# Kernel tuning notes

Measured on AMD Instinct MI355X. Metric: run time of the kernel, lower is better.

The kernel has to match this reference:

```python
import jax, jax.numpy as jnp
import numpy as np

NUM_LAYER = 6
NUM_HEADS = 1
NEG_INF = -1e9


def setup_inputs() -> dict:
    key = jax.random.key(0)
    ks = jax.random.split(key, 8)
    bs, C, N = 8, 128, 2048
    H0 = (jax.random.uniform(ks[0], (bs, N, N)) < 0.2).astype(jnp.float32)
    vertex_feat = jax.random.normal(ks[1], (bs, C, N), dtype=jnp.float32)
    edge_feat = jax.random.normal(ks[2], (bs, C, N), dtype=jnp.float32)
    s = 1.0 / np.sqrt(C)  # Conv1d(k=1) default init scale
    Wq = jax.random.uniform(ks[3], (C, C), minval=-s, maxval=s, dtype=jnp.float32)
    bq = jax.random.uniform(ks[4], (C,), minval=-s, maxval=s, dtype=jnp.float32)
    Wk = jax.random.uniform(ks[5], (C, C), minval=-s, maxval=s, dtype=jnp.float32)
    bk = jax.random.uniform(ks[6], (C,), minval=-s, maxval=s, dtype=jnp.float32)
    return {"H0": H0, "vertex_feat": vertex_feat, "edge_feat": edge_feat,
            "Wq": Wq, "bq": bq, "Wk": Wk, "bk": bk, "it": 4}


def reference(H0, vertex_feat, edge_feat, Wq, bq, Wk, bk, it):
    bs, N, _ = H0.shape
    C = Wq.shape[0]
    head = NUM_HEADS
    dh = C // head
    # Conv1d kernel_size=1 == pointwise linear over channel dim
    Q = (jnp.einsum('oc,bcn->bon', Wq, vertex_feat) + bq[None, :, None]).reshape(bs, head, dh, N)
    K = (jnp.einsum('oc,bcn->bon', Wk, edge_feat) + bk[None, :, None]).reshape(bs, head, dh, N)
    att = jnp.einsum('bhco,bhci->bhoi', Q, K) / np.sqrt(dh)  # [bs,h,N,N]
    mask = jnp.where(H0 > 0, 0.0, NEG_INF)                   # masked_fill(1-H0)
    score = jax.nn.sigmoid(att + mask[:, None]).sum(axis=1) / head  # [bs,N,N]
    # mask_score, choice='topk': keep top-k scores per row
    k = round(N * 0.1 * (NUM_LAYER - 1 - it))
    topk_vals = jax.lax.top_k(score, k)[0]          # [bs,N,k]
    a_min = topk_vals[..., -1:]                     # k-th largest per row
    W = jnp.where(score >= a_min, score, 0.0)
    H = jnp.where(W > 0, H0, 0.0)
    # degree-normalization matrices (diag_embed of 1/deg, inf -> 0)
    deg_E = H.sum(axis=1)   # [bs,N] edge degrees
    deg_V = H.sum(axis=2)   # [bs,N] vertex degrees
    De_n_1 = jax.vmap(jnp.diag)(jnp.where(deg_E != 0, 1.0 / deg_E, 0.0))
    Dv_n_1 = jax.vmap(jnp.diag)(jnp.where(deg_V != 0, 1.0 / deg_V, 0.0))
    # edge weights: L2-normalized column sums of W (F.normalize, eps=1e-12)
    W_edge = W.sum(axis=1)
    nrm = jnp.maximum(jnp.linalg.norm(W_edge, axis=1, keepdims=True), 1e-12)
    W_edge = (W_edge / nrm)[:, :, None]  # [bs,N,1]
    return H, W, De_n_1, Dv_n_1, W_edge
```

## Files before the change

### kernel.cpp

```cpp
#include <hip/hip_runtime.h>
#include <math.h>

#define NUM_LAYER 6

typedef __attribute__((ext_vector_type(8))) short short8;
typedef __attribute__((ext_vector_type(4))) float f32x4;
typedef unsigned short u16;

__device__ __forceinline__ void split3(float x, u16& h, u16& m, u16& l) {
  unsigned ux = __float_as_uint(x);
  h = (u16)(ux >> 16);
  float r1 = x - __uint_as_float(ux & 0xFFFF0000u);
  unsigned u1 = __float_as_uint(r1);
  m = (u16)(u1 >> 16);
  float r2 = r1 - __uint_as_float(u1 & 0xFFFF0000u);
  l = (u16)(__float_as_uint(r2) >> 16);
}

__global__ __launch_bounds__(256) void qk_gemm_split(
    const float* __restrict__ Wq, const float* __restrict__ bq,
    const float* __restrict__ vf,
    const float* __restrict__ Wk, const float* __restrict__ bk,
    const float* __restrict__ ef,
    u16* __restrict__ Qh, u16* __restrict__ Qm, u16* __restrict__ Ql,
    u16* __restrict__ Kh, u16* __restrict__ Km, u16* __restrict__ Kl,
    int C, int N, int bs) {
  int which = (int)blockIdx.y >= bs;
  int b = (int)blockIdx.y - (which ? bs : 0);
  const float* Wm = which ? Wk : Wq;
  const float* bias = which ? bk : bq;
  const float* X = (which ? ef : vf) + (size_t)b * C * N;
  u16* Ph = which ? Kh : Qh;
  u16* Pm = which ? Km : Qm;
  u16* Pl = which ? Kl : Ql;
  int n0 = blockIdx.x * 128;
  __shared__ float As[8][128];
  __shared__ float Xs[8][128];
  int t = threadIdx.x;
  int tx = t & 15, ty = t >> 4;
  int ao = t >> 1, ac = (t & 1) * 4;
  int lk = t >> 5, lj = (t & 31) * 4;
  float acc[8][8] = {};
  for (int c0 = 0; c0 < C; c0 += 8) {
    __syncthreads();
    float4 wv = *(const float4*)&Wm[(size_t)ao * C + c0 + ac];
    As[ac + 0][ao] = wv.x; As[ac + 1][ao] = wv.y;
    As[ac + 2][ao] = wv.z; As[ac + 3][ao] = wv.w;
    *(float4*)&Xs[lk][lj] = *(const float4*)&X[(size_t)(c0 + lk) * N + n0 + lj];
    __syncthreads();
#pragma unroll
    for (int kk = 0; kk < 8; ++kk) {
      float a[8], bb[8];
      *(float4*)&a[0]  = *(const float4*)&As[kk][ty * 4];
      *(float4*)&a[4]  = *(const float4*)&As[kk][64 + ty * 4];
      *(float4*)&bb[0] = *(const float4*)&Xs[kk][tx * 4];
      *(float4*)&bb[4] = *(const float4*)&Xs[kk][64 + tx * 4];
#pragma unroll
      for (int i = 0; i < 8; ++i)
#pragma unroll
        for (int j = 0; j < 8; ++j)
          acc[i][j] = fmaf(a[i], bb[j], acc[i][j]);
    }
  }
  float bv[8];
#pragma unroll
  for (int i = 0; i < 8; ++i) bv[i] = bias[(i >> 2) * 64 + ty * 4 + (i & 3)];
#pragma unroll
  for (int j = 0; j < 8; ++j) {
    int n = n0 + tx * 4 + (j & 3) + (j >> 2) * 64;
    size_t nb = ((size_t)b * N + n) * C;
#pragma unroll
    for (int g = 0; g < 2; ++g) {
      int r0 = g * 64 + ty * 4;
      ushort4 hv, mv, lv;
      split3(acc[g * 4 + 0][j] + bv[g * 4 + 0], hv.x, mv.x, lv.x);
      split3(acc[g * 4 + 1][j] + bv[g * 4 + 1], hv.y, mv.y, lv.y);
      split3(acc[g * 4 + 2][j] + bv[g * 4 + 2], hv.z, mv.z, lv.z);
      split3(acc[g * 4 + 3][j] + bv[g * 4 + 3], hv.w, mv.w, lv.w);
      *(ushort4*)&Ph[nb + r0] = hv;
      *(ushort4*)&Pm[nb + r0] = mv;
      *(ushort4*)&Pl[nb + r0] = lv;
    }
  }
}

__global__ __launch_bounds__(256) void att_mfma(
    const u16* __restrict__ Qh, const u16* __restrict__ Qm,
    const u16* __restrict__ Ql, const u16* __restrict__ Kh,
    const u16* __restrict__ Km, const u16* __restrict__ Kl,
    const float* __restrict__ H0, float* __restrict__ score,
    int C, int N, float rsdh) {
  int b = blockIdx.z;
  int o0 = blockIdx.y * 128, i0 = blockIdx.x * 128;
  __shared__ u16 sm[6][128][40];
  __shared__ float et[4][16][68];
  int t = threadIdx.x;
  int wave = t >> 6, lane = t & 63, quad = lane >> 4, lr = lane & 15;
  int wo = wave >> 1, wi = wave & 1;
  f32x4 acc[4][4];
#pragma unroll
  for (int mi = 0; mi < 4; ++mi)
#pragma unroll
    for (int ni = 0; ni < 4; ++ni) acc[mi][ni] = (f32x4){0.f, 0.f, 0.f, 0.f};

  int ro = t >> 1, ch = (t & 1) * 16;
  size_t qbase = ((size_t)b * N + o0 + ro) * C + ch;
  size_t kbase = ((size_t)b * N + i0 + ro) * C + ch;
  const u16* gq[3] = {Qh, Qm, Ql};
  const u16* gk[3] = {Kh, Km, Kl};

  for (int c0 = 0; c0 < C; c0 += 32) {
    __syncthreads();
#pragma unroll
    for (int a = 0; a < 3; ++a) {
      const uint4* src = (const uint4*)(gq[a] + qbase + c0);
      *(uint4*)&sm[a][ro][ch] = src[0];
      *(uint4*)&sm[a][ro][ch + 8] = src[1];
      const uint4* srk = (const uint4*)(gk[a] + kbase + c0);
      *(uint4*)&sm[3 + a][ro][ch] = srk[0];
      *(uint4*)&sm[3 + a][ro][ch + 8] = srk[1];
    }
    __syncthreads();
    short8 bh[4], bm[4], bl[4];
#pragma unroll
    for (int ni = 0; ni < 4; ++ni) {
      int row = wi * 64 + ni * 16 + lr;
      bh[ni] = *(const short8*)&sm[3][row][quad * 8];
      bm[ni] = *(const short8*)&sm[4][row][quad * 8];
      bl[ni] = *(const short8*)&sm[5][row][quad * 8];
    }
#pragma unroll
    for (int mi = 0; mi < 4; ++mi) {
      int row = wo * 64 + mi * 16 + lr;
      short8 ah = *(const short8*)&sm[0][row][quad * 8];
      short8 am = *(const short8*)&sm[1][row][quad * 8];
      short8 al = *(const short8*)&sm[2][row][quad * 8];
#pragma unroll
      for (int ni = 0; ni < 4; ++ni) {
        f32x4 c = acc[mi][ni];
        c = __builtin_amdgcn_mfma_f32_16x16x32_bf16(ah, bl[ni], c, 0, 0, 0);
        c = __builtin_amdgcn_mfma_f32_16x16x32_bf16(al, bh[ni], c, 0, 0, 0);
        c = __builtin_amdgcn_mfma_f32_16x16x32_bf16(am, bm[ni], c, 0, 0, 0);
        c = __builtin_amdgcn_mfma_f32_16x16x32_bf16(ah, bm[ni], c, 0, 0, 0);
        c = __builtin_amdgcn_mfma_f32_16x16x32_bf16(am, bh[ni], c, 0, 0, 0);
        c = __builtin_amdgcn_mfma_f32_16x16x32_bf16(ah, bh[ni], c, 0, 0, 0);
        acc[mi][ni] = c;
      }
    }
  }
  const float* Hb = H0 + (size_t)b * N * N;
  float* Sb = score + (size_t)b * N * N;
  int rr = lane >> 2, seg = lane & 3;
#pragma unroll
  for (int mi = 0; mi < 4; ++mi) {
#pragma unroll
    for (int ni = 0; ni < 4; ++ni)
#pragma unroll
      for (int r = 0; r < 4; ++r)
        et[wave][quad * 4 + r][ni * 16 + lr] = acc[mi][ni][r];
    __syncthreads();
    int o = o0 + wo * 64 + mi * 16 + rr;
    const float* hr = Hb + (size_t)o * N + i0 + wi * 64;
    float* sr = Sb + (size_t)o * N + i0 + wi * 64;
#pragma unroll
    for (int j = 0; j < 4; ++j) {
      int col = j * 16 + seg * 4;
      float4 c = *(const float4*)&et[wave][rr][col];
      float4 h = *(const float4*)&hr[col];
      float4 oV;
      oV.x = (h.x > 0.f) ? 1.f / (1.f + __expf(-c.x * rsdh)) : 0.f;
      oV.y = (h.y > 0.f) ? 1.f / (1.f + __expf(-c.y * rsdh)) : 0.f;
      oV.z = (h.z > 0.f) ? 1.f / (1.f + __expf(-c.z * rsdh)) : 0.f;
      oV.w = (h.w > 0.f) ? 1.f / (1.f + __expf(-c.w * rsdh)) : 0.f;
      *(float4*)&sr[col] = oV;
    }
    __syncthreads();
  }
}

template <int NQ>
__global__ __launch_bounds__(512) void select_wh_t(
    const float* __restrict__ H0, float* __restrict__ scoreW,
    float* __restrict__ Hout, float* __restrict__ degV,
    float* __restrict__ PE, float* __restrict__ PW,
    const int* __restrict__ itp, int N) {
  int b = blockIdx.y;
  int strip = blockIdx.x;
  int r0 = strip * 8;
  int t = threadIdx.x;
  int wave = t >> 6, lane = t & 63;
  size_t bNN = (size_t)b * N * N;
  __shared__ float aminS[8];
  __shared__ float dpart[8][8];

  {
    int row = r0 + wave;
    const float* srow = scoreW + bNN + (size_t)row * N;
    float v[NQ];
#pragma unroll
    for (int q = 0; q < NQ; ++q) v[q] = srow[lane + (q << 6)];
    int itv = *itp;
    int k = (int)floor((double)N * 0.1 * (double)(NUM_LAYER - 1 - itv) + 0.5);
    unsigned lo = 0u, hi = 0x3F800000u;
    while (lo < hi) {
      unsigned mid = lo + ((hi - lo + 1u) >> 1);
      float thr = __uint_as_float(mid);
      int c = 0;
#pragma unroll
      for (int q = 0; q < NQ; ++q) c += (v[q] >= thr) ? 1 : 0;
#pragma unroll
      for (int off = 1; off < 64; off <<= 1) c += __shfl_xor(c, off);
      if (c >= k) lo = mid; else hi = mid - 1u;
    }
    if (lane == 0) aminS[wave] = __uint_as_float(lo);
  }
  __syncthreads();

  float4 accE = {0.f, 0.f, 0.f, 0.f};
  float4 accW = {0.f, 0.f, 0.f, 0.f};
  float dv[8];
#pragma unroll
  for (int r = 0; r < 8; ++r) {
    float am = aminS[r];
    size_t off = bNN + (size_t)(r0 + r) * N + 4 * t;
    float4 s  = *(const float4*)(scoreW + off);
    float4 h0 = *(const float4*)(H0 + off);
    float4 w, h;
    w.x = (s.x >= am) ? s.x : 0.f; h.x = (w.x > 0.f) ? h0.x : 0.f;
    w.y = (s.y >= am) ? s.y : 0.f; h.y = (w.y > 0.f) ? h0.y : 0.f;
    w.z = (s.z >= am) ? s.z : 0.f; h.z = (w.z > 0.f) ? h0.z : 0.f;
    w.w = (s.w >= am) ? s.w : 0.f; h.w = (w.w > 0.f) ? h0.w : 0.f;
    *(float4*)(scoreW + off) = w;
    *(float4*)(Hout + off) = h;
    accW.x += w.x; accW.y += w.y; accW.z += w.z; accW.w += w.w;
    accE.x += h.x; accE.y += h.y; accE.z += h.z; accE.w += h.w;
    dv[r] = h.x + h.y + h.z + h.w;
  }
#pragma unroll
  for (int r = 0; r < 8; ++r) {
    float x = dv[r];
#pragma unroll
    for (int off = 32; off; off >>= 1) x += __shfl_down(x, off);
    if (lane == 0) dpart[wave][r] = x;
  }
  __syncthreads();
  if (t < 8) {
    float s = 0.f;
#pragma unroll
    for (int w = 0; w < 8; ++w) s += dpart[w][t];
    degV[b * N + r0 + t] = s;
  }
  int S = N >> 3;
  size_t pbase = ((size_t)b * S + strip) * N + 4 * t;
  *(float4*)(PE + pbase) = accE;
  *(float4*)(PW + pbase) = accW;
}

__global__ __launch_bounds__(256) void col_reduce(
    const float* __restrict__ PE, const float* __restrict__ PW,
    float* __restrict__ degE, float* __restrict__ We, int N, int S) {
  int b = blockIdx.y;
  int col = blockIdx.x * 256 + threadIdx.x;
  float se0 = 0.f, se1 = 0.f, sw0 = 0.f, sw1 = 0.f;
  for (int s = 0; s < S; s += 2) {
    size_t off0 = ((size_t)b * S + s) * N + col;
    size_t off1 = off0 + N;
    se0 += PE[off0]; se1 += PE[off1];
    sw0 += PW[off0]; sw1 += PW[off1];
  }
  degE[b * N + col] = se0 + se1;
  We[b * N + col] = sw0 + sw1;
}

__global__ __launch_bounds__(256) void dedv_fill(
    float* __restrict__ De, float* __restrict__ Dv,
    const float* __restrict__ degE, const float* __restrict__ degV, int N) {
  int arr = blockIdx.z;
  int b = blockIdx.y;
  int r0 = blockIdx.x * 8;
  float* out = (arr ? Dv : De) + (size_t)b * N * N;
  const float* deg = (arr ? degV : degE) + b * N;
  int t = threadIdx.x;
#pragma unroll
  for (int r = r0; r < r0 + 8; ++r) {
    float d = deg[r];
    float inv = (d != 0.f) ? 1.f / d : 0.f;
    size_t rowoff = (size_t)r * N;
    for (int c4 = t * 4; c4 < N; c4 += 1024) {
      float4 v = {0.f, 0.f, 0.f, 0.f};
      unsigned dd = (unsigned)(r - c4);
      if (dd < 4u) ((float*)&v)[dd] = inv;
      *(float4*)&out[rowoff + c4] = v;
    }
  }
}

__global__ __launch_bounds__(256) void wedge_norm(
    const float* __restrict__ We, float* __restrict__ out, int N) {
  int b = blockIdx.x;
  int t = threadIdx.x;
  const float* w = We + (size_t)b * N;
  float ss = 0.f;
  for (int i = t; i < N; i += 256) { float x = w[i]; ss += x * x; }
  for (int off = 32; off; off >>= 1) ss += __shfl_down(ss, off);
  __shared__ float p[4];
  if ((t & 63) == 0) p[t >> 6] = ss;
  __syncthreads();
  float tot = p[0] + p[1] + p[2] + p[3];
  float nrm = fmaxf(sqrtf(tot), 1e-12f);
  for (int i = t; i < N; i += 256) out[(size_t)b * N + i] = w[i] / nrm;
}

extern "C" void kernel_launch(void* const* d_in, const int* in_sizes, int n_in,
                              void* d_out, int out_size, void* d_ws, size_t ws_size,
                              hipStream_t stream) {
  const float* H0 = (const float*)d_in[0];
  const float* vf = (const float*)d_in[1];
  const float* ef = (const float*)d_in[2];
  const float* Wq = (const float*)d_in[3];
  const float* bq = (const float*)d_in[4];
  const float* Wk = (const float*)d_in[5];
  const float* bk = (const float*)d_in[6];
  const int* itp  = (const int*)d_in[7];

  int C = (int)(sqrt((double)in_sizes[3]) + 0.5);
  long long ratio = (long long)in_sizes[0] / in_sizes[1];
  int N = (int)(C * ratio);
  int bs = (int)(in_sizes[1] / ((long long)C * N));
  size_t bNN = (size_t)bs * N * N;
  size_t bNC = (size_t)bs * N * C;
  int S = N >> 3;
  size_t pElems = (size_t)bs * S * N;

  float* outH  = (float*)d_out;
  float* outW  = outH + bNN;
  float* outDe = outW + bNN;
  float* outDv = outDe + bNN;
  float* outWe = outDv + bNN;

  size_t bsN = (size_t)bs * N;
  float* degE = (float*)d_ws;
  float* degV = degE + bsN;
  float* We   = degV + bsN;
  u16* splits;
  float* PE;
  float* PW;
  size_t need = 3 * bsN * sizeof(float) + 6 * bNC * sizeof(u16) +
                2 * pElems * sizeof(float);
  if (ws_size >= need) {
    splits = (u16*)(We + bsN);
    PE = (float*)(splits + 6 * bNC);
    PW = PE + pElems;
  } else {
    splits = (u16*)outDe;
    PE = outDv;
    PW = PE + pElems;
  }
  u16* Qh = splits;
  u16* Qm = Qh + bNC;
  u16* Ql = Qm + bNC;
  u16* Kh = Ql + bNC;
  u16* Km = Kh + bNC;
  u16* Kl = Km + bNC;

  float rsdh = (float)(1.0 / sqrt((double)C));

  qk_gemm_split<<<dim3(N / 128, 2 * bs), 256, 0, stream>>>(
      Wq, bq, vf, Wk, bk, ef, Qh, Qm, Ql, Kh, Km, Kl, C, N, bs);
  att_mfma<<<dim3(N / 128, N / 128, bs), 256, 0, stream>>>(
      Qh, Qm, Ql, Kh, Km, Kl, H0, outW, C, N, rsdh);
  if (N == 2048)
    select_wh_t<32><<<dim3(S, bs), 512, 0, stream>>>(H0, outW, outH, degV,
                                                     PE, PW, itp, N);
  else if (N == 1024)
    select_wh_t<16><<<dim3(S, bs), 512, 0, stream>>>(H0, outW, outH, degV,
                                                     PE, PW, itp, N);
  else
    select_wh_t<64><<<dim3(S, bs), 512, 0, stream>>>(H0, outW, outH, degV,
                                                     PE, PW, itp, N);
  col_reduce<<<dim3(N / 256, bs), 256, 0, stream>>>(PE, PW, degE, We, N, S);
  dedv_fill<<<dim3(N / 8, bs, 2), 256, 0, stream>>>(outDe, outDv, degE,
                                                    degV, N);
  wedge_norm<<<dim3(bs), 256, 0, stream>>>(We, outWe, N);
}
```

Before: 918.6 us.

## Split top-k threshold from selection pass and load MFMA operands directly from global

The attention kernel now loads the Q/K bf16 split operands straight from global memory into registers and drops the shared-memory staging and its two barriers per k-step. It relies on L1/L2 for reuse, at the cost of more redundant global traffic. The fused select kernel is split in two: a top-k threshold kernel that writes per-row minima, and a streaming 256-thread select kernel that handles 16 rows per block with G float4 groups. This halves the number of column partials and adjusts col_reduce to match, aiming to separate the latency-bound bisection from the bandwidth-bound streaming pass. The score matrix is read twice in exchange.

```diff
diff --git a/kernel.cpp b/kernel.cpp
--- a/kernel.cpp
+++ b/kernel.cpp
@@ -84,7 +84,7 @@
   }
 }
 
-__global__ __launch_bounds__(256) void att_mfma(
+__global__ __launch_bounds__(256) void att_mfma_reg(
     const u16* __restrict__ Qh, const u16* __restrict__ Qm,
     const u16* __restrict__ Ql, const u16* __restrict__ Kh,
     const u16* __restrict__ Km, const u16* __restrict__ Kl,
@@ -92,7 +92,6 @@
     int C, int N, float rsdh) {
   int b = blockIdx.z;
   int o0 = blockIdx.y * 128, i0 = blockIdx.x * 128;
-  __shared__ u16 sm[6][128][40];
   __shared__ float et[4][16][68];
   int t = threadIdx.x;
   int wave = t >> 6, lane = t & 63, quad = lane >> 4, lr = lane & 15;
@@ -103,38 +102,25 @@
 #pragma unroll
     for (int ni = 0; ni < 4; ++ni) acc[mi][ni] = (f32x4){0.f, 0.f, 0.f, 0.f};
 
-  int ro = t >> 1, ch = (t & 1) * 16;
-  size_t qbase = ((size_t)b * N + o0 + ro) * C + ch;
-  size_t kbase = ((size_t)b * N + i0 + ro) * C + ch;
-  const u16* gq[3] = {Qh, Qm, Ql};
-  const u16* gk[3] = {Kh, Km, Kl};
+  unsigned qoff = (unsigned)(b * N + o0 + wo * 64 + lr) * C + quad * 8;
+  unsigned koff = (unsigned)(b * N + i0 + wi * 64 + lr) * C + quad * 8;
+  unsigned rstep = 16u * C;
 
   for (int c0 = 0; c0 < C; c0 += 32) {
-    __syncthreads();
-#pragma unroll
-    for (int a = 0; a < 3; ++a) {
-      const uint4* src = (const uint4*)(gq[a] + qbase + c0);
-      *(uint4*)&sm[a][ro][ch] = src[0];
-      *(uint4*)&sm[a][ro][ch + 8] = src[1];
-      const uint4* srk = (const uint4*)(gk[a] + kbase + c0);
-      *(uint4*)&sm[3 + a][ro][ch] = srk[0];
-      *(uint4*)&sm[3 + a][ro][ch + 8] = srk[1];
-    }
-    __syncthreads();
     short8 bh[4], bm[4], bl[4];
 #pragma unroll
     for (int ni = 0; ni < 4; ++ni) {
-      int row = wi * 64 + ni * 16 + lr;
-      bh[ni] = *(const short8*)&sm[3][row][quad * 8];
-      bm[ni] = *(const short8*)&sm[4][row][quad * 8];
-      bl[ni] = *(const short8*)&sm[5][row][quad * 8];
+      unsigned o = koff + ni * rstep + c0;
+      bh[ni] = *(const short8*)&Kh[o];
+      bm[ni] = *(const short8*)&Km[o];
+      bl[ni] = *(const short8*)&Kl[o];
     }
 #pragma unroll
     for (int mi = 0; mi < 4; ++mi) {
-      int row = wo * 64 + mi * 16 + lr;
-      short8 ah = *(const short8*)&sm[0][row][quad * 8];
-      short8 am = *(const short8*)&sm[1][row][quad * 8];
-      short8 al = *(const short8*)&sm[2][row][quad * 8];
+      unsigned o = qoff + mi * rstep + c0;
+      short8 ah = *(const short8*)&Qh[o];
+      short8 am = *(const short8*)&Qm[o];
+      short8 al = *(const short8*)&Ql[o];
 #pragma unroll
       for (int ni = 0; ni < 4; ++ni) {
         f32x4 c = acc[mi][ni];
@@ -179,81 +165,92 @@
 }
 
 template <int NQ>
-__global__ __launch_bounds__(512) void select_wh_t(
-    const float* __restrict__ H0, float* __restrict__ scoreW,
-    float* __restrict__ Hout, float* __restrict__ degV,
-    float* __restrict__ PE, float* __restrict__ PW,
+__global__ __launch_bounds__(512) void topk_amin(
+    const float* __restrict__ score, float* __restrict__ amin,
     const int* __restrict__ itp, int N) {
   int b = blockIdx.y;
+  int row = blockIdx.x * 8 + (threadIdx.x >> 6);
+  int lane = threadIdx.x & 63;
+  const float* srow = score + ((size_t)b * N + row) * N;
+  float v[NQ];
+#pragma unroll
+  for (int q = 0; q < NQ; ++q) v[q] = srow[lane + (q << 6)];
+  int itv = *itp;
+  int k = (int)floor((double)N * 0.1 * (double)(NUM_LAYER - 1 - itv) + 0.5);
+  unsigned lo = 0u, hi = 0x3F800000u;
+  while (lo < hi) {
+    unsigned mid = lo + ((hi - lo + 1u) >> 1);
+    float thr = __uint_as_float(mid);
+    int c = 0;
+#pragma unroll
+    for (int q = 0; q < NQ; ++q) c += (v[q] >= thr) ? 1 : 0;
+#pragma unroll
+    for (int off = 1; off < 64; off <<= 1) c += __shfl_xor(c, off);
+    if (c >= k) lo = mid; else hi = mid - 1u;
+  }
+  if (lane == 0) amin[b * N + row] = __uint_as_float(lo);
+}
+
+template <int G>
+__global__ __launch_bounds__(256) void select_stream(
+    const float* __restrict__ H0, float* __restrict__ scoreW,
+    float* __restrict__ Hout, const float* __restrict__ amin,
+    float* __restrict__ degV, float* __restrict__ PE, float* __restrict__ PW,
+    int N) {
+  int b = blockIdx.y;
   int strip = blockIdx.x;
-  int r0 = strip * 8;
+  int r0 = strip * 16;
   int t = threadIdx.x;
   int wave = t >> 6, lane = t & 63;
   size_t bNN = (size_t)b * N * N;
-  __shared__ float aminS[8];
-  __shared__ float dpart[8][8];
-
-  {
-    int row = r0 + wave;
-    const float* srow = scoreW + bNN + (size_t)row * N;
-    float v[NQ];
-#pragma unroll
-    for (int q = 0; q < NQ; ++q) v[q] = srow[lane + (q << 6)];
-    int itv = *itp;
-    int k = (int)floor((double)N * 0.1 * (double)(NUM_LAYER - 1 - itv) + 0.5);
-    unsigned lo = 0u, hi = 0x3F800000u;
-    while (lo < hi) {
-      unsigned mid = lo + ((hi - lo + 1u) >> 1);
-      float thr = __uint_as_float(mid);
-      int c = 0;
-#pragma unroll
-      for (int q = 0; q < NQ; ++q) c += (v[q] >= thr) ? 1 : 0;
-#pragma unroll
-      for (int off = 1; off < 64; off <<= 1) c += __shfl_xor(c, off);
-      if (c >= k) lo = mid; else hi = mid - 1u;
-    }
-    if (lane == 0) aminS[wave] = __uint_as_float(lo);
-  }
-  __syncthreads();
-
-  float4 accE = {0.f, 0.f, 0.f, 0.f};
-  float4 accW = {0.f, 0.f, 0.f, 0.f};
-  float dv[8];
-#pragma unroll
-  for (int r = 0; r < 8; ++r) {
-    float am = aminS[r];
-    size_t off = bNN + (size_t)(r0 + r) * N + 4 * t;
-    float4 s  = *(const float4*)(scoreW + off);
-    float4 h0 = *(const float4*)(H0 + off);
-    float4 w, h;
-    w.x = (s.x >= am) ? s.x : 0.f; h.x = (w.x > 0.f) ? h0.x : 0.f;
-    w.y = (s.y >= am) ? s.y : 0.f; h.y = (w.y > 0.f) ? h0.y : 0.f;
-    w.z = (s.z >= am) ? s.z : 0.f; h.z = (w.z > 0.f) ? h0.z : 0.f;
-    w.w = (s.w >= am) ? s.w : 0.f; h.w = (w.w > 0.f) ? h0.w : 0.f;
-    *(float4*)(scoreW + off) = w;
-    *(float4*)(Hout + off) = h;
-    accW.x += w.x; accW.y += w.y; accW.z += w.z; accW.w += w.w;
-    accE.x += h.x; accE.y += h.y; accE.z += h.z; accE.w += h.w;
-    dv[r] = h.x + h.y + h.z + h.w;
-  }
-#pragma unroll
-  for (int r = 0; r < 8; ++r) {
+  float4 accE[G], accW[G];
+#pragma unroll
+  for (int g = 0; g < G; ++g) {
+    accE[g] = (float4){0.f, 0.f, 0.f, 0.f};
+    accW[g] = (float4){0.f, 0.f, 0.f, 0.f};
+  }
+  __shared__ float dpart[4][16];
+  float dv[16];
+#pragma unroll
+  for (int r = 0; r < 16; ++r) {
+    float am = amin[b * N + r0 + r];
+    size_t rowoff = bNN + (size_t)(r0 + r) * N + 4 * t;
+    float rs = 0.f;
+#pragma unroll
+    for (int g = 0; g < G; ++g) {
+      size_t off = rowoff + g * 1024;
+      float4 s  = *(const float4*)(scoreW + off);
+      float4 h0 = *(const float4*)(H0 + off);
+      float4 w, h;
+      w.x = (s.x >= am) ? s.x : 0.f; h.x = (w.x > 0.f) ? h0.x : 0.f;
+      w.y = (s.y >= am) ? s.y : 0.f; h.y = (w.y > 0.f) ? h0.y : 0.f;
+      w.z = (s.z >= am) ? s.z : 0.f; h.z = (w.z > 0.f) ? h0.z : 0.f;
+      w.w = (s.w >= am) ? s.w : 0.f; h.w = (w.w > 0.f) ? h0.w : 0.f;
+      *(float4*)(scoreW + off) = w;
+      *(float4*)(Hout + off) = h;
+      accW[g].x += w.x; accW[g].y += w.y; accW[g].z += w.z; accW[g].w += w.w;
+      accE[g].x += h.x; accE[g].y += h.y; accE[g].z += h.z; accE[g].w += h.w;
+      rs += h.x + h.y + h.z + h.w;
+    }
+    dv[r] = rs;
+  }
+#pragma unroll
+  for (int r = 0; r < 16; ++r) {
     float x = dv[r];
 #pragma unroll
     for (int off = 32; off; off >>= 1) x += __shfl_down(x, off);
     if (lane == 0) dpart[wave][r] = x;
   }
   __syncthreads();
-  if (t < 8) {
-    float s = 0.f;
-#pragma unroll
-    for (int w = 0; w < 8; ++w) s += dpart[w][t];
-    degV[b * N + r0 + t] = s;
-  }
-  int S = N >> 3;
+  if (t < 16)
+    degV[b * N + r0 + t] = dpart[0][t] + dpart[1][t] + dpart[2][t] + dpart[3][t];
+  int S = N >> 4;
   size_t pbase = ((size_t)b * S + strip) * N + 4 * t;
-  *(float4*)(PE + pbase) = accE;
-  *(float4*)(PW + pbase) = accW;
+#pragma unroll
+  for (int g = 0; g < G; ++g) {
+    *(float4*)(PE + pbase + g * 1024) = accE[g];
+    *(float4*)(PW + pbase + g * 1024) = accW[g];
+  }
 }
 
 __global__ __launch_bounds__(256) void col_reduce(
@@ -262,11 +259,12 @@
   int b = blockIdx.y;
   int col = blockIdx.x * 256 + threadIdx.x;
   float se0 = 0.f, se1 = 0.f, sw0 = 0.f, sw1 = 0.f;
-  for (int s = 0; s < S; s += 2) {
-    size_t off0 = ((size_t)b * S + s) * N + col;
-    size_t off1 = off0 + N;
-    se0 += PE[off0]; se1 += PE[off1];
-    sw0 += PW[off0]; sw1 += PW[off1];
+  for (int s = 0; s < S; s += 4) {
+    size_t o0 = ((size_t)b * S + s) * N + col;
+    se0 += PE[o0];           sw0 += PW[o0];
+    se1 += PE[o0 + N];       sw1 += PW[o0 + N];
+    se0 += PE[o0 + 2 * (size_t)N]; sw0 += PW[o0 + 2 * (size_t)N];
+    se1 += PE[o0 + 3 * (size_t)N]; sw1 += PW[o0 + 3 * (size_t)N];
   }
   degE[b * N + col] = se0 + se1;
   We[b * N + col] = sw0 + sw1;
@@ -329,7 +327,7 @@
   int bs = (int)(in_sizes[1] / ((long long)C * N));
   size_t bNN = (size_t)bs * N * N;
   size_t bNC = (size_t)bs * N * C;
-  int S = N >> 3;
+  int S = N >> 4;
   size_t pElems = (size_t)bs * S * N;
 
   float* outH  = (float*)d_out;
@@ -339,13 +337,14 @@
   float* outWe = outDv + bNN;
 
   size_t bsN = (size_t)bs * N;
-  float* degE = (float*)d_ws;
+  float* amin = (float*)d_ws;
+  float* degE = amin + bsN;
   float* degV = degE + bsN;
   float* We   = degV + bsN;
   u16* splits;
   float* PE;
   float* PW;
-  size_t need = 3 * bsN * sizeof(float) + 6 * bNC * sizeof(u16) +
+  size_t need = 4 * bsN * sizeof(float) + 6 * bNC * sizeof(u16) +
                 2 * pElems * sizeof(float);
   if (ws_size >= need) {
     splits = (u16*)(We + bsN);
@@ -367,17 +366,21 @@
 
   qk_gemm_split<<<dim3(N / 128, 2 * bs), 256, 0, stream>>>(
       Wq, bq, vf, Wk, bk, ef, Qh, Qm, Ql, Kh, Km, Kl, C, N, bs);
-  att_mfma<<<dim3(N / 128, N / 128, bs), 256, 0, stream>>>(
+  att_mfma_reg<<<dim3(N / 128, N / 128, bs), 256, 0, stream>>>(
       Qh, Qm, Ql, Kh, Km, Kl, H0, outW, C, N, rsdh);
-  if (N == 2048)
-    select_wh_t<32><<<dim3(S, bs), 512, 0, stream>>>(H0, outW, outH, degV,
-                                                     PE, PW, itp, N);
-  else if (N == 1024)
-    select_wh_t<16><<<dim3(S, bs), 512, 0, stream>>>(H0, outW, outH, degV,
-                                                     PE, PW, itp, N);
-  else
-    select_wh_t<64><<<dim3(S, bs), 512, 0, stream>>>(H0, outW, outH, degV,
-                                                     PE, PW, itp, N);
+  if (N == 2048) {
+    topk_amin<32><<<dim3(N / 8, bs), 512, 0, stream>>>(outW, amin, itp, N);
+    select_stream<2><<<dim3(S, bs), 256, 0, stream>>>(H0, outW, outH, amin,
+                                                      degV, PE, PW, N);
+  } else if (N == 1024) {
+    topk_amin<16><<<dim3(N / 8, bs), 512, 0, stream>>>(outW, amin, itp, N);
+    select_stream<1><<<dim3(S, bs), 256, 0, stream>>>(H0, outW, outH, amin,
+                                                      degV, PE, PW, N);
+  } else {
+    topk_amin<64><<<dim3(N / 8, bs), 512, 0, stream>>>(outW, amin, itp, N);
+    select_stream<4><<<dim3(S, bs), 256, 0, stream>>>(H0, outW, outH, amin,
+                                                      degV, PE, PW, N);
+  }
   col_reduce<<<dim3(N / 256, bs), 256, 0, stream>>>(PE, PW, degE, We, N, S);
   dedv_fill<<<dim3(N / 8, bs, 2), 256, 0, stream>>>(outDe, outDv, degE,
                                                     degV, N);
```

Measured after the change: 967.8 us. 1.05x slower.

## Keep score row in registers and accumulate column sums via LDS atomics

Applied to the files above, without the earlier changes.

The top-k select kernel now loads each row's scores once as float4 registers and reuses them for thresholding, where before the strip was read again from global memory. Each wave handles one full row, so the per-column edge-degree and weight partial sums are gathered with shared-memory atomicAdd into a block-wide column buffer, then written out per strip. The col_reduce loop is unrolled by four. This trades a second global read for many LDS atomics, which may contend, and it adds dynamic shared memory that could lower occupancy.

```diff
diff --git a/kernel.cpp b/kernel.cpp
--- a/kernel.cpp
+++ b/kernel.cpp
@@ -178,82 +178,82 @@
   }
 }
 
-template <int NQ>
-__global__ __launch_bounds__(512) void select_wh_t(
+template <int V4>
+__global__ __launch_bounds__(512) void topk_select(
     const float* __restrict__ H0, float* __restrict__ scoreW,
     float* __restrict__ Hout, float* __restrict__ degV,
     float* __restrict__ PE, float* __restrict__ PW,
     const int* __restrict__ itp, int N) {
   int b = blockIdx.y;
   int strip = blockIdx.x;
-  int r0 = strip * 8;
   int t = threadIdx.x;
   int wave = t >> 6, lane = t & 63;
+  int row = strip * 8 + wave;
   size_t bNN = (size_t)b * N * N;
-  __shared__ float aminS[8];
-  __shared__ float dpart[8][8];
-
-  {
-    int row = r0 + wave;
-    const float* srow = scoreW + bNN + (size_t)row * N;
-    float v[NQ];
-#pragma unroll
-    for (int q = 0; q < NQ; ++q) v[q] = srow[lane + (q << 6)];
-    int itv = *itp;
-    int k = (int)floor((double)N * 0.1 * (double)(NUM_LAYER - 1 - itv) + 0.5);
-    unsigned lo = 0u, hi = 0x3F800000u;
-    while (lo < hi) {
-      unsigned mid = lo + ((hi - lo + 1u) >> 1);
-      float thr = __uint_as_float(mid);
-      int c = 0;
-#pragma unroll
-      for (int q = 0; q < NQ; ++q) c += (v[q] >= thr) ? 1 : 0;
-#pragma unroll
-      for (int off = 1; off < 64; off <<= 1) c += __shfl_xor(c, off);
-      if (c >= k) lo = mid; else hi = mid - 1u;
-    }
-    if (lane == 0) aminS[wave] = __uint_as_float(lo);
-  }
+  size_t rowoff = bNN + (size_t)row * N;
+  extern __shared__ float cols[];
+  float* colE = cols;
+  float* colW = cols + N;
+  for (int i = t; i < 2 * N; i += 512) cols[i] = 0.f;
+
+  float4 v4[V4];
+#pragma unroll
+  for (int q = 0; q < V4; ++q)
+    v4[q] = *(const float4*)(scoreW + rowoff + 4 * lane + (q << 8));
+  int itv = *itp;
+  int k = (int)floor((double)N * 0.1 * (double)(NUM_LAYER - 1 - itv) + 0.5);
+  unsigned lo = 0u, hi = 0x3F800000u;
+  while (lo < hi) {
+    unsigned mid = lo + ((hi - lo + 1u) >> 1);
+    float thr = __uint_as_float(mid);
+    int c = 0;
+#pragma unroll
+    for (int q = 0; q < V4; ++q) {
+      c += (v4[q].x >= thr) ? 1 : 0;
+      c += (v4[q].y >= thr) ? 1 : 0;
+      c += (v4[q].z >= thr) ? 1 : 0;
+      c += (v4[q].w >= thr) ? 1 : 0;
+    }
+#pragma unroll
+    for (int off = 1; off < 64; off <<= 1) c += __shfl_xor(c, off);
+    if (c >= k) lo = mid; else hi = mid - 1u;
+  }
+  float am = __uint_as_float(lo);
   __syncthreads();
 
-  float4 accE = {0.f, 0.f, 0.f, 0.f};
-  float4 accW = {0.f, 0.f, 0.f, 0.f};
-  float dv[8];
-#pragma unroll
-  for (int r = 0; r < 8; ++r) {
-    float am = aminS[r];
-    size_t off = bNN + (size_t)(r0 + r) * N + 4 * t;
-    float4 s  = *(const float4*)(scoreW + off);
-    float4 h0 = *(const float4*)(H0 + off);
+  float rs = 0.f;
+#pragma unroll
+  for (int q = 0; q < V4; ++q) {
+    int c0 = 4 * lane + (q << 8);
+    float4 s = v4[q];
+    float4 h0 = *(const float4*)(H0 + rowoff + c0);
     float4 w, h;
     w.x = (s.x >= am) ? s.x : 0.f; h.x = (w.x > 0.f) ? h0.x : 0.f;
     w.y = (s.y >= am) ? s.y : 0.f; h.y = (w.y > 0.f) ? h0.y : 0.f;
     w.z = (s.z >= am) ? s.z : 0.f; h.z = (w.z > 0.f) ? h0.z : 0.f;
     w.w = (s.w >= am) ? s.w : 0.f; h.w = (w.w > 0.f) ? h0.w : 0.f;
-    *(float4*)(scoreW + off) = w;
-    *(float4*)(Hout + off) = h;
-    accW.x += w.x; accW.y += w.y; accW.z += w.z; accW.w += w.w;
-    accE.x += h.x; accE.y += h.y; accE.z += h.z; accE.w += h.w;
-    dv[r] = h.x + h.y + h.z + h.w;
-  }
-#pragma unroll
-  for (int r = 0; r < 8; ++r) {
-    float x = dv[r];
-#pragma unroll
-    for (int off = 32; off; off >>= 1) x += __shfl_down(x, off);
-    if (lane == 0) dpart[wave][r] = x;
-  }
+    *(float4*)(scoreW + rowoff + c0) = w;
+    *(float4*)(Hout + rowoff + c0) = h;
+    rs += h.x + h.y + h.z + h.w;
+    if (h.x != 0.f) atomicAdd(&colE[c0 + 0], h.x);
+    if (h.y != 0.f) atomicAdd(&colE[c0 + 1], h.y);
+    if (h.z != 0.f) atomicAdd(&colE[c0 + 2], h.z);
+    if (h.w != 0.f) atomicAdd(&colE[c0 + 3], h.w);
+    if (w.x != 0.f) atomicAdd(&colW[c0 + 0], w.x);
+    if (w.y != 0.f) atomicAdd(&colW[c0 + 1], w.y);
+    if (w.z != 0.f) atomicAdd(&colW[c0 + 2], w.z);
+    if (w.w != 0.f) atomicAdd(&colW[c0 + 3], w.w);
+  }
+#pragma unroll
+  for (int off = 32; off; off >>= 1) rs += __shfl_down(rs, off);
+  if (lane == 0) degV[b * N + row] = rs;
   __syncthreads();
-  if (t < 8) {
-    float s = 0.f;
-#pragma unroll
-    for (int w = 0; w < 8; ++w) s += dpart[w][t];
-    degV[b * N + r0 + t] = s;
-  }
   int S = N >> 3;
-  size_t pbase = ((size_t)b * S + strip) * N + 4 * t;
-  *(float4*)(PE + pbase) = accE;
-  *(float4*)(PW + pbase) = accW;
+  size_t pbase = ((size_t)b * S + strip) * N;
+  for (int c = 4 * t; c < N; c += 2048) {
+    *(float4*)(PE + pbase + c) = *(const float4*)&colE[c];
+    *(float4*)(PW + pbase + c) = *(const float4*)&colW[c];
+  }
 }
 
 __global__ __launch_bounds__(256) void col_reduce(
@@ -262,11 +262,12 @@
   int b = blockIdx.y;
   int col = blockIdx.x * 256 + threadIdx.x;
   float se0 = 0.f, se1 = 0.f, sw0 = 0.f, sw1 = 0.f;
-  for (int s = 0; s < S; s += 2) {
-    size_t off0 = ((size_t)b * S + s) * N + col;
-    size_t off1 = off0 + N;
-    se0 += PE[off0]; se1 += PE[off1];
-    sw0 += PW[off0]; sw1 += PW[off1];
+  for (int s = 0; s < S; s += 4) {
+    size_t o0 = ((size_t)b * S + s) * N + col;
+    se0 += PE[o0];           sw0 += PW[o0];
+    se1 += PE[o0 + N];       sw1 += PW[o0 + N];
+    se0 += PE[o0 + 2 * (size_t)N]; sw0 += PW[o0 + 2 * (size_t)N];
+    se1 += PE[o0 + 3 * (size_t)N]; sw1 += PW[o0 + 3 * (size_t)N];
   }
   degE[b * N + col] = se0 + se1;
   We[b * N + col] = sw0 + sw1;
@@ -364,20 +365,21 @@
   u16* Kl = Km + bNC;
 
   float rsdh = (float)(1.0 / sqrt((double)C));
+  size_t colsBytes = 2 * (size_t)N * sizeof(float);
 
   qk_gemm_split<<<dim3(N / 128, 2 * bs), 256, 0, stream>>>(
       Wq, bq, vf, Wk, bk, ef, Qh, Qm, Ql, Kh, Km, Kl, C, N, bs);
   att_mfma<<<dim3(N / 128, N / 128, bs), 256, 0, stream>>>(
       Qh, Qm, Ql, Kh, Km, Kl, H0, outW, C, N, rsdh);
   if (N == 2048)
-    select_wh_t<32><<<dim3(S, bs), 512, 0, stream>>>(H0, outW, outH, degV,
-                                                     PE, PW, itp, N);
+    topk_select<8><<<dim3(S, bs), 512, colsBytes, stream>>>(
+        H0, outW, outH, degV, PE, PW, itp, N);
   else if (N == 1024)
-    select_wh_t<16><<<dim3(S, bs), 512, 0, stream>>>(H0, outW, outH, degV,
-                                                     PE, PW, itp, N);
+    topk_select<4><<<dim3(S, bs), 512, colsBytes, stream>>>(
+        H0, outW, outH, degV, PE, PW, itp, N);
   else
-    select_wh_t<64><<<dim3(S, bs), 512, 0, stream>>>(H0, outW, outH, degV,
-                                                     PE, PW, itp, N);
+    topk_select<16><<<dim3(S, bs), 512, colsBytes, stream>>>(
+        H0, outW, outH, degV, PE, PW, itp, N);
   col_reduce<<<dim3(N / 256, bs), 256, 0, stream>>>(PE, PW, degE, We, N, S);
   dedv_fill<<<dim3(N / 8, bs, 2), 256, 0, stream>>>(outDe, outDv, degE,
                                                     degV, N);
```

Result: faster. 879.1 us (-4.3%).
